# Kernel optimization log

Hardware: AMD Instinct MI355X
Metric: run time of the kernel (lower is better)

## Reference

```python
import jax, jax.numpy as jnp
import numpy as np

B, T, Tc = 64, 256, 16
VW, VC, L = 100000, 128, 25
CE, CH = 25, 25          # char embed / char lstm hidden per direction
WE, WH = 100, 100        # word embed / word lstm hidden per direction (bi -> 200)
DW = WE + 2 * CH         # 150, word-LSTM input dim


def lstm(x, Wih, Whh, b):
    """Unidirectional LSTM over time axis 1. x: [N, S, D] -> [N, S, H]. PyTorch gate order i,f,g,o."""
    N = x.shape[0]
    H = Whh.shape[0]
    x_t = jnp.swapaxes(x, 0, 1)  # [S, N, D]

    def step(carry, xt):
        h, c = carry
        g = xt @ Wih + h @ Whh + b
        i, f, gg, o = jnp.split(g, 4, axis=-1)
        c = jax.nn.sigmoid(f) * c + jax.nn.sigmoid(i) * jnp.tanh(gg)
        h = jax.nn.sigmoid(o) * jnp.tanh(c)
        return (h, c), h

    h0 = jnp.zeros((N, H), x.dtype)
    _, hs = jax.lax.scan(step, (h0, h0), x_t)
    return jnp.swapaxes(hs, 0, 1)  # [N, S, H]


def crf_nll(em, tags, trans, start, end):
    """Negative log-likelihood of linear-chain CRF (no mask; full-length sequences)."""
    # gold path score
    em_score = jnp.take_along_axis(em, tags[:, :, None], axis=2).squeeze(-1).sum(axis=1)
    tr_score = trans[tags[:, :-1], tags[:, 1:]].sum(axis=1)
    gold = start[tags[:, 0]] + em_score + tr_score + end[tags[:, -1]]
    # forward algorithm (log partition)
    alpha0 = start[None, :] + em[:, 0]  # [B, L]

    def step(alpha, e_t):
        # alpha: [B, L] prev-tag scores; trans: [L, L]; e_t: [B, L]
        new = jax.nn.logsumexp(alpha[:, :, None] + trans[None, :, :] + e_t[:, None, :], axis=1)
        return new, None

    alpha, _ = jax.lax.scan(step, alpha0, jnp.swapaxes(em[:, 1:], 0, 1))
    logZ = jax.nn.logsumexp(alpha + end[None, :], axis=1)
    return jnp.sum(logZ - gold)


def setup_inputs():
    key = jax.random.key(0)
    ks = jax.random.split(key, 24)
    f = lambda i, shape: jax.random.normal(ks[i], shape, jnp.float32) * 0.1
    return {
        "tok_tensor": jax.random.randint(ks[0], (B, T), 0, VW),
        "tag_tensor": jax.random.randint(ks[1], (B, T), 0, L),
        "lengths": jnp.full((B,), T, jnp.int32),
        "char_tensor": jax.random.randint(ks[2], (B * T, Tc), 0, VC),
        "char_lengths": jax.random.randint(ks[3], (B * T,), 1, Tc + 1),
        "char_tensor_recover": jax.random.permutation(ks[4], B * T),
        "word_emb": f(5, (VW, WE)),
        "char_emb": f(6, (VC, CE)),
        "cWih_f": f(7, (CE, 4 * CH)), "cWhh_f": f(8, (CH, 4 * CH)), "cb_f": jnp.zeros((4 * CH,), jnp.float32),
        "cWih_b": f(9, (CE, 4 * CH)), "cWhh_b": f(10, (CH, 4 * CH)), "cb_b": jnp.zeros((4 * CH,), jnp.float32),
        "wWih_f": f(11, (DW, 4 * WH)), "wWhh_f": f(12, (WH, 4 * WH)), "wb_f": jnp.zeros((4 * WH,), jnp.float32),
        "wWih_b": f(13, (DW, 4 * WH)), "wWhh_b": f(14, (WH, 4 * WH)), "wb_b": jnp.zeros((4 * WH,), jnp.float32),
        "W_tag": f(15, (2 * WH, L)), "b_tag": jnp.zeros((L,), jnp.float32),
        "trans": f(16, (L, L)), "start": f(17, (L,)), "end": f(18, (L,)),
    }


def reference(tok_tensor, tag_tensor, lengths, char_tensor, char_lengths, char_tensor_recover,
              word_emb, char_emb,
              cWih_f, cWhh_f, cb_f, cWih_b, cWhh_b, cb_b,
              wWih_f, wWhh_f, wb_f, wWih_b, wWhh_b, wb_b,
              W_tag, b_tag, trans, start, end):
    N = char_tensor.shape[0]  # B*T words
    # ---- char BiLSTM: last hidden of each direction per word ----
    ce = char_emb[char_tensor]                      # [N, Tc, CE]
    last = char_lengths - 1
    hf = lstm(ce, cWih_f, cWhh_f, cb_f)             # [N, Tc, CH]
    h_fwd = hf[jnp.arange(N), last]                 # forward last valid hidden
    # backward: reverse each word within its length, scan, take hidden at step len-1
    t_ar = jnp.arange(Tc)[None, :]
    rev_idx = jnp.where(t_ar < char_lengths[:, None], char_lengths[:, None] - 1 - t_ar, t_ar)
    ce_rev = jnp.take_along_axis(ce, rev_idx[:, :, None], axis=1)
    hb = lstm(ce_rev, cWih_b, cWhh_b, cb_b)
    h_bwd = hb[jnp.arange(N), last]
    char_feat = jnp.concatenate([h_fwd, h_bwd], axis=-1)[char_tensor_recover].reshape(B, T, 2 * CH)
    # ---- concat word + char features (dropout = identity in eval) ----
    x = jnp.concatenate([word_emb[tok_tensor], char_feat], axis=-1)  # [B, T, DW]
    # ---- word BiLSTM (full-length sequences) ----
    h_f = lstm(x, wWih_f, wWhh_f, wb_f)
    h_b = jnp.flip(lstm(jnp.flip(x, axis=1), wWih_b, wWhh_b, wb_b), axis=1)
    seq = jnp.concatenate([h_f, h_b], axis=-1)       # [B, T, 2*WH]
    # ---- emissions + CRF NLL ----
    em = seq @ W_tag + b_tag                         # [B, T, L]
    return crf_nll(em, tag_tensor, trans, start, end)
```

## Files before the change

kernel.cpp:

```cpp
#include <hip/hip_runtime.h>
#include <hip/hip_bf16.h>

#define NB 64
#define NT 256
#define TC 16
#define NL 25
#define NWORDS 16384
#define DWd 150
#define WEd 100
#define WPB 5

__device__ __forceinline__ float sigf(float x){ return __fdividef(1.f, 1.f + __expf(-x)); }
__device__ __forceinline__ float tanhf_(float x){
    float ax = fabsf(x);
    float e = __expf(-2.f*ax);
    float r = (1.f - e) * __fdividef(1.f, 1.f + e);
    return copysignf(r, x);
}
__device__ __forceinline__ float RL(float v, int k){
    return __int_as_float(__builtin_amdgcn_readlane(__float_as_int(v), k));
}

__global__ void k_zero(int* __restrict__ meta){
  if (threadIdx.x < 34) meta[threadIdx.x] = 0;
}
__global__ __launch_bounds__(256) void k_hist(const int* __restrict__ char_lengths,
                                              int* __restrict__ hist){
  __shared__ int lh[16];
  int tid = threadIdx.x;
  if (tid < 16) lh[tid] = 0;
  __syncthreads();
  int w = blockIdx.x*256 + tid;
  atomicAdd(&lh[char_lengths[w]-1], 1);
  __syncthreads();
  if (tid < 16) atomicAdd(&hist[tid], lh[tid]);
}
__global__ void k_scan(const int* __restrict__ hist, int* __restrict__ cursor){
  if (threadIdx.x == 0){
    int acc = 0;
    for (int i=0;i<16;i++){ cursor[i] = acc; acc += hist[i]; }
  }
}
__global__ __launch_bounds__(256) void k_scatter(const int* __restrict__ char_lengths,
                                                 int* __restrict__ cursor,
                                                 int* __restrict__ widx){
  __shared__ int lh[16], lbase[16];
  int tid = threadIdx.x;
  if (tid < 16) lh[tid] = 0;
  __syncthreads();
  int w = blockIdx.x*256 + tid;
  int len = char_lengths[w]-1;
  int lrank = atomicAdd(&lh[len], 1);
  __syncthreads();
  if (tid < 16) lbase[tid] = atomicAdd(&cursor[tid], lh[tid]);
  __syncthreads();
  widx[lbase[len] + lrank] = w;
}

__global__ void k_gxc(const float* __restrict__ char_emb,
                      const float* __restrict__ cWih_f, const float* __restrict__ cb_f,
                      const float* __restrict__ cWih_b, const float* __restrict__ cb_b,
                      float* __restrict__ gxc){
  int i = blockIdx.x*blockDim.x + threadIdx.x;
  if (i >= 128*2*100) return;
  int col = i % 100; int d = (i/100) & 1; int c = i/200;
  const float* Wih = d ? cWih_b : cWih_f;
  const float* bb  = d ? cb_b  : cb_f;
  float acc = bb[col];
  #pragma unroll
  for (int k=0;k<25;k++) acc += char_emb[c*25+k]*Wih[k*100+col];
  gxc[i] = acc;
}

__global__ __launch_bounds__(512) void k_char(const int* __restrict__ char_tensor,
   const int* __restrict__ char_lengths, const int* __restrict__ widx,
   const float* __restrict__ cWhh_f, const float* __restrict__ cWhh_b,
   const float* __restrict__ gxc, float* __restrict__ cf){
  __shared__ float h_lds[2][WPB][28];
  __shared__ int   chars[WPB][TC];
  __shared__ int   lens[WPB];
  __shared__ int   wids[WPB];
  int tid = threadIdx.x;
  int d  = blockIdx.x & 1;
  int wb = blockIdx.x >> 1;
  int w0 = wb*WPB;
  if (tid < WPB){
    int slot = w0 + tid; if (slot > NWORDS-1) slot = NWORDS-1;
    wids[tid] = widx[slot];
  }
  __syncthreads();
  if (tid < WPB*TC){
    int ww = wids[tid/TC];
    chars[tid/TC][tid%TC] = char_tensor[ww*TC + (tid%TC)];
  }
  if (tid < WPB) lens[tid] = char_lengths[wids[tid]];
  if (tid < 2*WPB*28){
    int p = tid/(WPB*28); int rr = tid - p*WPB*28;
    h_lds[p][rr/28][rr%28] = 0.f;
  }
  int wsub = tid/100;
  int r    = tid - wsub*100;
  int u    = r >> 2;
  int gid  = r & 3;
  bool gate_thr = tid < WPB*100;
  int col = gid*25 + u;
  const float* Wh = d ? cWhh_b : cWhh_f;
  float wcol[25];
  if (gate_thr){
    #pragma unroll
    for (int k=0;k<25;k++) wcol[k] = Wh[k*100 + col];
  }
  float c_reg = 0.f, h_last = 0.f;
  __syncthreads();
  int lmax = lens[0];
  #pragma unroll
  for (int q=1;q<WPB;q++) lmax = max(lmax, lens[q]);
  int len = gate_thr ? lens[wsub] : 1;
  bool isg = (gid == 2);
  float gnext = 0.f;
  if (gate_thr){
    int ci = d ? (len-1) : 0;
    if (ci < 0 || ci >= TC) ci = 0;
    gnext = gxc[(size_t)(chars[wsub][ci]*2+d)*100 + col];
  }
  for (int t=0;t<lmax;t++){
    float gcur = gnext;
    if (gate_thr && t+1 < TC){
      int ci = d ? (len-2-t) : (t+1);
      if (ci < 0 || ci >= TC) ci = 0;
      gnext = gxc[(size_t)(chars[wsub][ci]*2+d)*100 + col];
    }
    float x = 0.f;
    if (gate_thr){
      float a0 = gcur, a1 = 0.f, a2 = 0.f, a3 = 0.f;
      const float4* h4 = (const float4*)h_lds[t&1][wsub];
      #pragma unroll
      for (int kq=0;kq<6;kq++){
        float4 hq = h4[kq];
        a0 += hq.x*wcol[4*kq];
        a1 += hq.y*wcol[4*kq+1];
        a2 += hq.z*wcol[4*kq+2];
        a3 += hq.w*wcol[4*kq+3];
      }
      a0 += h_lds[t&1][wsub][24]*wcol[24];
      float a = (a0+a1)+(a2+a3);
      x = isg ? tanhf_(a) : sigf(a);
    }
    float A = __shfl_xor(x, 1, 64);
    float B = __shfl_xor(x, 2, 64);
    float C = __shfl_xor(B, 1, 64);
    if (gate_thr && gid == 0){
      float hv;
      if (t < len){
        c_reg = A*c_reg + x*B;
        hv = C*tanhf_(c_reg);
        h_last = hv;
      } else hv = h_last;
      h_lds[(t+1)&1][wsub][u] = hv;
    }
    __syncthreads();
  }
  if (gate_thr && gid == 0){
    int w = wids[wsub];
    cf[(size_t)w*56 + d*28 + u] = h_last;
  }
}

__global__ __launch_bounds__(256) void k_wih(const int* __restrict__ tok,
    const int* __restrict__ recover,
    const float* __restrict__ word_emb, const float* __restrict__ cf,
    const float* __restrict__ Wf, const float* __restrict__ bf,
    const float* __restrict__ Wb, const float* __restrict__ bbias,
    float* __restrict__ gx){
  __shared__ float As[150][72];
  __shared__ int toks[64], recs[64];
  int tid = threadIdx.x;
  int m0 = (blockIdx.x>>2)*64;
  int nt = blockIdx.x & 3;
  int n0 = nt*256;
  if (tid < 64) toks[tid] = tok[m0 + tid];
  else if (tid < 128) recs[tid-64] = recover[m0 + tid - 64];
  __syncthreads();
  for (int i=tid; i<64*150; i+=256){
    int r = i/150; int k = i - r*150;
    float v;
    if (k < WEd) v = word_emb[(long)toks[r]*WEd + k];
    else {
      int ci = k - WEd;
      int dd = ci/25; int uu = ci - dd*25;
      v = cf[(size_t)recs[r]*56 + dd*28 + uu];
    }
    As[k][r] = v;
  }
  __syncthreads();
  int tn = tid & 31; int tm = tid >> 5;
  int j0 = n0 + tn*8;
  bool colok = j0 < 800;
  int d = (j0 >= 400) ? 1 : 0;
  const float* W = d ? Wb : Wf;
  int jc = j0 - d*400;
  float acc[8][8];
  #pragma unroll
  for (int mi=0;mi<8;mi++)
    #pragma unroll
    for (int ni=0;ni<8;ni++) acc[mi][ni]=0.f;
  if (colok){
    for (int k=0;k<150;k++){
      float4 b0 = *(const float4*)&W[k*400 + jc];
      float4 b1 = *(const float4*)&W[k*400 + jc + 4];
      float4 a0 = *(const float4*)&As[k][tm*8];
      float4 a1 = *(const float4*)&As[k][tm*8+4];
      float av[8] = {a0.x,a0.y,a0.z,a0.w,a1.x,a1.y,a1.z,a1.w};
      float bv[8] = {b0.x,b0.y,b0.z,b0.w,b1.x,b1.y,b1.z,b1.w};
      #pragma unroll
      for (int mi=0;mi<8;mi++)
        #pragma unroll
        for (int ni=0;ni<8;ni++) acc[mi][ni] += av[mi]*bv[ni];
    }
    const float* bptr = d ? bbias : bf;
    float bias[8];
    #pragma unroll
    for (int ni=0;ni<8;ni++) bias[ni] = bptr[jc+ni];
    #pragma unroll
    for (int mi=0;mi<8;mi++){
      int p = m0 + tm*8 + mi;
      float* orow = gx + ((long)d*NWORDS + p)*400 + jc;
      #pragma unroll
      for (int ni=0;ni<8;ni++) orow[ni] = acc[mi][ni] + bias[ni];
    }
  }
}

__global__ __launch_bounds__(448, 2) void k_wlstm(const float* __restrict__ gx,
     const float* __restrict__ Whf, const float* __restrict__ Whb,
     float* __restrict__ hseq){
  __shared__ float wstage[10000];
  __shared__ float h_lds[100];
  __shared__ float act[400];
  int tid = threadIdx.x;
  int s = blockIdx.x & 63; int d = blockIdx.x >> 6;
  const float* Wh = d ? Whb : Whf;
  int j = tid;
  bool colthr = j < 400;
  float wreg[100];
  #pragma unroll
  for (int ch=0; ch<4; ch++){
    for (int i=tid; i<2500; i+=448)
      ((float4*)wstage)[i] = ((const float4*)(Wh + ch*10000))[i];
    __syncthreads();
    if (colthr){
      #pragma unroll
      for (int kk=0;kk<25;kk++) wreg[ch*25+kk] = wstage[kk*400 + j];
    }
    __syncthreads();
  }
  if (tid < 100) h_lds[tid] = 0.f;
  float c_reg = 0.f;
  const float* gxd = gx + ((long)d*NWORDS + (long)s*256)*400;
  bool isg = (j >= 200) && (j < 300);
  __syncthreads();
  float gnext = 0.f;
  if (colthr) gnext = gxd[(d?255:0)*400 + j];
  for (int t=0;t<256;t++){
    float gcur = gnext;
    if (colthr && t+1 < 256){
      int tn = d ? (255-(t+1)) : (t+1);
      gnext = gxd[tn*400 + j];
    }
    if (colthr){
      float a0 = gcur, a1 = 0.f, a2 = 0.f, a3 = 0.f;
      const float4* h4 = (const float4*)h_lds;
      #pragma unroll
      for (int kq=0;kq<25;kq++){
        float4 hq = h4[kq];
        a0 += hq.x*wreg[4*kq];
        a1 += hq.y*wreg[4*kq+1];
        a2 += hq.z*wreg[4*kq+2];
        a3 += hq.w*wreg[4*kq+3];
      }
      float a = (a0+a1)+(a2+a3);
      act[j] = isg ? tanhf_(a) : sigf(a);
    }
    __syncthreads();
    if (tid < 100){
      float si = act[tid], sf = act[100+tid], sg = act[200+tid], so = act[300+tid];
      c_reg = sf*c_reg + si*sg;
      float hv = so*tanhf_(c_reg);
      h_lds[tid] = hv;
      int ttc = d ? (255-t) : t;
      hseq[((long)d*NWORDS + s*256 + ttc)*100 + tid] = hv;
    }
    __syncthreads();
  }
}

__global__ __launch_bounds__(256) void k_em(const float* __restrict__ hseq,
    const float* __restrict__ Wtag, const float* __restrict__ btag,
    float* __restrict__ em){
  __shared__ float hrow[8][200];
  __shared__ float WsT[25][204];
  int tid = threadIdx.x;
  for (int i=tid;i<5000;i+=256){
    int c = i/200; int k = i - c*200;
    WsT[c][k] = Wtag[k*25 + c];
  }
  int p0 = blockIdx.x*8;
  for (int i=tid;i<8*200;i+=256){
    int r = i/200; int k = i - r*200;
    int p = p0+r;
    hrow[r][k] = (k<100) ? hseq[(long)p*100+k] : hseq[((long)NWORDS + p)*100 + (k-100)];
  }
  __syncthreads();
  int r = tid>>5; int c = tid&31;
  if (c<25){
    float a0=0.f,a1=0.f,a2=0.f,a3=0.f;
    #pragma unroll 10
    for (int k=0;k<200;k+=4){
      float4 h4 = *(const float4*)&hrow[r][k];
      float4 w4 = *(const float4*)&WsT[c][k];
      a0 += h4.x*w4.x; a1 += h4.y*w4.y;
      a2 += h4.z*w4.z; a3 += h4.w*w4.w;
    }
    em[(long)(p0+r)*25 + c] = btag[c] + (a0+a1)+(a2+a3);
  }
}

__global__ __launch_bounds__(64) void k_crf(const float* __restrict__ em,
    const int* __restrict__ tag, const float* __restrict__ trans,
    const float* __restrict__ start, const float* __restrict__ endv,
    float* __restrict__ part){
  int s = blockIdx.x;
  int lane = threadIdx.x;
  const float* emb = em + (long)s*256*25;
  float etr[25];
  #pragma unroll
  for (int k=0;k<25;k++) etr[k] = (lane<25) ? __expf(trans[k*25+lane]) : 0.f;
  float alpha = (lane<25) ? (start[lane] + emb[lane]) : 0.f;
  float enext = (lane<25) ? emb[25+lane] : 0.f;
  for (int t=1;t<256;t++){
    float ecur = enext;
    if (t<255 && lane<25) enext = emb[(t+1)*25 + lane];
    float base = RL(alpha, 0);
    float e = __expf(alpha - base);
    float s0=0.f,s1=0.f,s2=0.f,s3=0.f,s4=0.f;
    #pragma unroll
    for (int k=0;k<5;k++) s0 += RL(e,k)    * etr[k];
    #pragma unroll
    for (int k=0;k<5;k++) s1 += RL(e,5+k)  * etr[5+k];
    #pragma unroll
    for (int k=0;k<5;k++) s2 += RL(e,10+k) * etr[10+k];
    #pragma unroll
    for (int k=0;k<5;k++) s3 += RL(e,15+k) * etr[15+k];
    #pragma unroll
    for (int k=0;k<5;k++) s4 += RL(e,20+k) * etr[20+k];
    float ssum = ((s0+s1)+(s2+s3))+s4;
    alpha = __logf(ssum) + base + ecur;
  }
  float val = (lane<25) ? (alpha + endv[lane]) : -1e30f;
  float m2 = -1e30f;
  #pragma unroll
  for (int k=0;k<25;k++) m2 = fmaxf(m2, RL(val,k));
  float s2s = 0.f;
  #pragma unroll
  for (int k=0;k<25;k++) s2s += __expf(RL(val,k) - m2);
  float logZ = __logf(s2s) + m2;
  const int* tg = tag + s*256;
  float gp = 0.f;
  for (int t=lane; t<256; t+=64){
    int a = tg[t];
    gp += emb[t*25 + a];
    if (t<255) gp += trans[a*25 + tg[t+1]];
  }
  #pragma unroll
  for (int off=32; off; off>>=1) gp += __shfl_xor(gp, off, 64);
  if (lane==0){
    float gold = gp + start[tg[0]] + endv[tg[255]];
    part[s] = logZ - gold;
  }
}

__global__ __launch_bounds__(64) void k_red(const float* __restrict__ part, float* __restrict__ out){
  float v = part[threadIdx.x];
  #pragma unroll
  for (int off=32; off; off>>=1) v += __shfl_xor(v, off, 64);
  if (threadIdx.x==0) out[0] = v;
}

extern "C" void kernel_launch(void* const* d_in, const int* in_sizes, int n_in,
                              void* d_out, int out_size, void* d_ws, size_t ws_size,
                              hipStream_t stream){
  const int* tok          = (const int*)d_in[0];
  const int* tagp         = (const int*)d_in[1];
  const int* char_tensor  = (const int*)d_in[3];
  const int* char_lengths = (const int*)d_in[4];
  const int* recover      = (const int*)d_in[5];
  const float* word_emb = (const float*)d_in[6];
  const float* char_emb = (const float*)d_in[7];
  const float* cWih_f=(const float*)d_in[8];  const float* cWhh_f=(const float*)d_in[9];  const float* cb_f=(const float*)d_in[10];
  const float* cWih_b=(const float*)d_in[11]; const float* cWhh_b=(const float*)d_in[12]; const float* cb_b=(const float*)d_in[13];
  const float* wWih_f=(const float*)d_in[14]; const float* wWhh_f=(const float*)d_in[15]; const float* wb_f=(const float*)d_in[16];
  const float* wWih_b=(const float*)d_in[17]; const float* wWhh_b=(const float*)d_in[18]; const float* wb_b=(const float*)d_in[19];
  const float* W_tag=(const float*)d_in[20];  const float* b_tag=(const float*)d_in[21];
  const float* trans=(const float*)d_in[22];  const float* startv=(const float*)d_in[23]; const float* endv=(const float*)d_in[24];

  float* ws  = (float*)d_ws;
  float* gxc = ws;
  float* cf  = ws + 25600;
  float* gx  = ws + 943104;
  float* hseq= ws + 14050304;
  float* em  = ws;
  float* part= ws + 17327104;
  int*   meta= (int*)(ws + 17327168);
  int*   widx= meta + 64;
  float* out = (float*)d_out;

  k_zero   <<<1,   64,  0, stream>>>(meta);
  k_gxc    <<<100, 256, 0, stream>>>(char_emb, cWih_f, cb_f, cWih_b, cb_b, gxc);
  k_hist   <<<64,  256, 0, stream>>>(char_lengths, meta);
  k_scan   <<<1,   64,  0, stream>>>(meta, meta+16);
  k_scatter<<<64,  256, 0, stream>>>(char_lengths, meta+16, widx);
  k_char   <<<6554,512, 0, stream>>>(char_tensor, char_lengths, widx, cWhh_f, cWhh_b, gxc, cf);
  k_wih    <<<1024,256, 0, stream>>>(tok, recover, word_emb, cf, wWih_f, wb_f, wWih_b, wb_b, gx);
  k_wlstm  <<<128, 448, 0, stream>>>(gx, wWhh_f, wWhh_b, hseq);
  k_em     <<<2048,256, 0, stream>>>(hseq, W_tag, b_tag, em);
  k_crf    <<<64,  64,  0, stream>>>(em, tagp, trans, startv, endv, part);
  k_red    <<<1,   64,  0, stream>>>(part, out);
}
```

Before: 521.7 us.

## Interleave LSTM gate columns per lane and combine via shuffles, double-buffer hidden state

The word-LSTM recurrence now maps the four gates of each hidden unit to four adjacent lanes. The gates are combined with cross-lane xor shuffles instead of going through an LDS activation buffer. The hidden state is double-buffered, which removes one of the two block barriers per timestep. Separately, the meta zeroing is folded into k_gxc, which drops one kernel launch. The risk is more shuffle instructions per step and the correctness of the double-buffer ordering.

```diff
diff --git a/kernel.cpp b/kernel.cpp
--- a/kernel.cpp
+++ b/kernel.cpp
@@ -21,47 +21,12 @@
     return __int_as_float(__builtin_amdgcn_readlane(__float_as_int(v), k));
 }
 
-__global__ void k_zero(int* __restrict__ meta){
-  if (threadIdx.x < 34) meta[threadIdx.x] = 0;
-}
-__global__ __launch_bounds__(256) void k_hist(const int* __restrict__ char_lengths,
-                                              int* __restrict__ hist){
-  __shared__ int lh[16];
-  int tid = threadIdx.x;
-  if (tid < 16) lh[tid] = 0;
-  __syncthreads();
-  int w = blockIdx.x*256 + tid;
-  atomicAdd(&lh[char_lengths[w]-1], 1);
-  __syncthreads();
-  if (tid < 16) atomicAdd(&hist[tid], lh[tid]);
-}
-__global__ void k_scan(const int* __restrict__ hist, int* __restrict__ cursor){
-  if (threadIdx.x == 0){
-    int acc = 0;
-    for (int i=0;i<16;i++){ cursor[i] = acc; acc += hist[i]; }
-  }
-}
-__global__ __launch_bounds__(256) void k_scatter(const int* __restrict__ char_lengths,
-                                                 int* __restrict__ cursor,
-                                                 int* __restrict__ widx){
-  __shared__ int lh[16], lbase[16];
-  int tid = threadIdx.x;
-  if (tid < 16) lh[tid] = 0;
-  __syncthreads();
-  int w = blockIdx.x*256 + tid;
-  int len = char_lengths[w]-1;
-  int lrank = atomicAdd(&lh[len], 1);
-  __syncthreads();
-  if (tid < 16) lbase[tid] = atomicAdd(&cursor[tid], lh[tid]);
-  __syncthreads();
-  widx[lbase[len] + lrank] = w;
-}
-
 __global__ void k_gxc(const float* __restrict__ char_emb,
                       const float* __restrict__ cWih_f, const float* __restrict__ cb_f,
                       const float* __restrict__ cWih_b, const float* __restrict__ cb_b,
-                      float* __restrict__ gxc){
+                      float* __restrict__ gxc, int* __restrict__ meta){
   int i = blockIdx.x*blockDim.x + threadIdx.x;
+  if (blockIdx.x == 0 && threadIdx.x < 34) meta[threadIdx.x] = 0;
   if (i >= 128*2*100) return;
   int col = i % 100; int d = (i/100) & 1; int c = i/200;
   const float* Wih = d ? cWih_b : cWih_f;
@@ -70,6 +35,39 @@
   #pragma unroll
   for (int k=0;k<25;k++) acc += char_emb[c*25+k]*Wih[k*100+col];
   gxc[i] = acc;
+}
+
+__global__ __launch_bounds__(256) void k_hist(const int* __restrict__ char_lengths,
+                                              int* __restrict__ hist){
+  __shared__ int lh[16];
+  int tid = threadIdx.x;
+  if (tid < 16) lh[tid] = 0;
+  __syncthreads();
+  int w = blockIdx.x*256 + tid;
+  atomicAdd(&lh[char_lengths[w]-1], 1);
+  __syncthreads();
+  if (tid < 16) atomicAdd(&hist[tid], lh[tid]);
+}
+__global__ void k_scan(const int* __restrict__ hist, int* __restrict__ cursor){
+  if (threadIdx.x == 0){
+    int acc = 0;
+    for (int i=0;i<16;i++){ cursor[i] = acc; acc += hist[i]; }
+  }
+}
+__global__ __launch_bounds__(256) void k_scatter(const int* __restrict__ char_lengths,
+                                                 int* __restrict__ cursor,
+                                                 int* __restrict__ widx){
+  __shared__ int lh[16], lbase[16];
+  int tid = threadIdx.x;
+  if (tid < 16) lh[tid] = 0;
+  __syncthreads();
+  int w = blockIdx.x*256 + tid;
+  int len = char_lengths[w]-1;
+  int lrank = atomicAdd(&lh[len], 1);
+  __syncthreads();
+  if (tid < 16) lbase[tid] = atomicAdd(&cursor[tid], lh[tid]);
+  __syncthreads();
+  widx[lbase[len] + lrank] = w;
 }
 
 __global__ __launch_bounds__(512) void k_char(const int* __restrict__ char_tensor,
@@ -235,13 +233,14 @@
      const float* __restrict__ Whf, const float* __restrict__ Whb,
      float* __restrict__ hseq){
   __shared__ float wstage[10000];
-  __shared__ float h_lds[100];
-  __shared__ float act[400];
+  __shared__ float h_lds[2][100];
   int tid = threadIdx.x;
   int s = blockIdx.x & 63; int d = blockIdx.x >> 6;
   const float* Wh = d ? Whb : Whf;
-  int j = tid;
-  bool colthr = j < 400;
+  int u   = tid >> 2;
+  int gid = tid & 3;
+  bool colthr = tid < 400;
+  int col = gid*100 + u;
   float wreg[100];
   #pragma unroll
   for (int ch=0; ch<4; ch++){
@@ -250,26 +249,27 @@
     __syncthreads();
     if (colthr){
       #pragma unroll
-      for (int kk=0;kk<25;kk++) wreg[ch*25+kk] = wstage[kk*400 + j];
+      for (int kk=0;kk<25;kk++) wreg[ch*25+kk] = wstage[kk*400 + col];
     }
     __syncthreads();
   }
-  if (tid < 100) h_lds[tid] = 0.f;
+  if (tid < 200) h_lds[tid/100][tid%100] = 0.f;
   float c_reg = 0.f;
   const float* gxd = gx + ((long)d*NWORDS + (long)s*256)*400;
-  bool isg = (j >= 200) && (j < 300);
+  bool isg = (gid == 2);
   __syncthreads();
   float gnext = 0.f;
-  if (colthr) gnext = gxd[(d?255:0)*400 + j];
+  if (colthr) gnext = gxd[(d?255:0)*400 + col];
   for (int t=0;t<256;t++){
     float gcur = gnext;
     if (colthr && t+1 < 256){
       int tn = d ? (255-(t+1)) : (t+1);
-      gnext = gxd[tn*400 + j];
-    }
+      gnext = gxd[tn*400 + col];
+    }
+    float x = 0.f;
     if (colthr){
       float a0 = gcur, a1 = 0.f, a2 = 0.f, a3 = 0.f;
-      const float4* h4 = (const float4*)h_lds;
+      const float4* h4 = (const float4*)h_lds[t&1];
       #pragma unroll
       for (int kq=0;kq<25;kq++){
         float4 hq = h4[kq];
@@ -279,16 +279,17 @@
         a3 += hq.w*wreg[4*kq+3];
       }
       float a = (a0+a1)+(a2+a3);
-      act[j] = isg ? tanhf_(a) : sigf(a);
-    }
-    __syncthreads();
-    if (tid < 100){
-      float si = act[tid], sf = act[100+tid], sg = act[200+tid], so = act[300+tid];
-      c_reg = sf*c_reg + si*sg;
-      float hv = so*tanhf_(c_reg);
-      h_lds[tid] = hv;
+      x = isg ? tanhf_(a) : sigf(a);
+    }
+    float A = __shfl_xor(x, 1, 64);
+    float B = __shfl_xor(x, 2, 64);
+    float C = __shfl_xor(B, 1, 64);
+    if (colthr && gid == 0){
+      c_reg = A*c_reg + x*B;
+      float hv = C*tanhf_(c_reg);
+      h_lds[(t+1)&1][u] = hv;
       int ttc = d ? (255-t) : t;
-      hseq[((long)d*NWORDS + s*256 + ttc)*100 + tid] = hv;
+      hseq[((long)d*NWORDS + s*256 + ttc)*100 + u] = hv;
     }
     __syncthreads();
   }
@@ -414,8 +415,7 @@
   int*   widx= meta + 64;
   float* out = (float*)d_out;
 
-  k_zero   <<<1,   64,  0, stream>>>(meta);
-  k_gxc    <<<100, 256, 0, stream>>>(char_emb, cWih_f, cb_f, cWih_b, cb_b, gxc);
+  k_gxc    <<<100, 256, 0, stream>>>(char_emb, cWih_f, cb_f, cWih_b, cb_b, gxc, meta);
   k_hist   <<<64,  256, 0, stream>>>(char_lengths, meta);
   k_scan   <<<1,   64,  0, stream>>>(meta, meta+16);
   k_scatter<<<64,  256, 0, stream>>>(char_lengths, meta+16, widx);
```

Result: no change. 525.7 us (+0.8%).
